# Kernel tuning notes

Hardware: AMD Instinct MI355X
Metric: run time of the kernel (lower is better)

The kernel has to match this reference:

```python
import jax, jax.numpy as jnp
import numpy as np

H, W = 512, 512
N_GAUSS = 4096
T_EPS = 1e-3          # early-termination threshold from the torch loop
COV_DIAG = 25.0       # hardcoded cov_2d = eye(2) * 25 in rasterize_gaussians


def quat_to_rot(q):
    # standard (w, x, y, z) quaternion -> rotation matrix, with normalization
    q = q / jnp.linalg.norm(q)
    w, x, y, z = q[0], q[1], q[2], q[3]
    return jnp.array([
        [1 - 2 * (y * y + z * z), 2 * (x * y - w * z),     2 * (x * z + w * y)],
        [2 * (x * y + w * z),     1 - 2 * (x * x + z * z), 2 * (y * z - w * x)],
        [2 * (x * z - w * y),     2 * (y * z + w * x),     1 - 2 * (x * x + y * y)],
    ])


def setup_inputs() -> dict:
    key = jax.random.key(0)
    k0, k1, k2, k3 = jax.random.split(key, 4)
    xy = jax.random.uniform(k0, (N_GAUSS, 2), minval=-2.0, maxval=2.0)
    z = jax.random.uniform(k1, (N_GAUSS, 1), minval=4.0, maxval=10.0)
    positions = jnp.concatenate([xy, z], axis=-1)                    # [N,3], z>0
    colors = jax.random.uniform(k2, (N_GAUSS, 3))                    # [N,3] in [0,1]
    opacities = jax.random.uniform(k3, (N_GAUSS,)) * 0.5             # [N]
    quaternion = jnp.array([1.0, 0.05, 0.02, 0.01], dtype=jnp.float32)
    cam_position = jnp.zeros(3, dtype=jnp.float32)
    intrinsics = jnp.array([[500.0, 0.0, 256.0],
                            [0.0, 500.0, 256.0],
                            [0.0, 0.0, 1.0]], dtype=jnp.float32)
    background_color = jnp.zeros(3, dtype=jnp.float32)
    return {"positions": positions, "colors": colors, "opacities": opacities,
            "quaternion": quaternion, "cam_position": cam_position,
            "intrinsics": intrinsics, "background_color": background_color}


def _render(positions, colors, opacities, quaternion, cam_position, intrinsics,
            background_color):
    R = quat_to_rot(quaternion)                                      # [3,3]
    pos_cam = (positions - cam_position[None, :]) @ R.T              # [N,3]
    proj = pos_cam @ intrinsics.T                                    # [N,3]
    screen = proj[:, :2] / proj[:, 2:3]                              # [N,2]
    depths = proj[:, 2]                                              # [N]

    order = jnp.argsort(-depths)                                     # back-to-front
    centers_s = screen[order]
    colors_s = colors[order]
    opac_s = opacities[order]
    depth_s = pos_cam[order, 2]

    yy, xx = jnp.meshgrid(jnp.arange(H, dtype=jnp.float32),
                          jnp.arange(W, dtype=jnp.float32), indexing="ij")
    pix = jnp.stack([xx, yy], axis=-1)                               # [H,W,2] (x,y)

    init_color = jnp.broadcast_to(background_color[:, None, None], (3, H, W))
    carry0 = (init_color, jnp.zeros((H, W)), jnp.zeros((H, W)), jnp.ones((H, W)))

    def step(carry, g):
        color_acc, depth_acc, alpha_acc, T = carry
        center, color, opacity, depth = g
        # emulate the `if transmittance.max() < 1e-3: break` exactly: once T
        # saturates it is monotone, so masking all later contributions == break
        active = (jnp.max(T) >= T_EPS).astype(T.dtype)
        diff = pix - center[None, None, :]                           # [H,W,2]
        mahal = jnp.sum(diff * diff, axis=-1) / COV_DIAG             # cov_inv = I/25
        alpha = jnp.clip(jnp.exp(-0.5 * mahal) * opacity, 0.0, 1.0) * active
        ta = T * alpha
        color_acc = color_acc + ta[None, :, :] * color[:, None, None]
        depth_acc = depth_acc + ta * depth
        alpha_acc = alpha_acc + ta
        T = T * (1.0 - alpha)
        return (color_acc, depth_acc, alpha_acc, T), None

    (image, depth_map, alpha_map, _), _ = jax.lax.scan(
        step, carry0, (centers_s, colors_s, opac_s, depth_s))
    return image, depth_map, alpha_map


def reference(positions, colors, opacities, quaternion, cam_position, intrinsics,
              background_color):
    return _render(positions, colors, opacities, quaternion, cam_position,
                   intrinsics, background_color)
```

## Files before the change

kernel.cpp:

```cpp
#include <hip/hip_runtime.h>
#include <hip/hip_bf16.h>

#define N_GAUSS 4096
#define H 512
#define W 512
#define HW (H * W)

#define SEG 4
#define GSEG (N_GAUSS / SEG)
#define NSUB (GSEG / 64)
#define CULL2 1444.0f
#define CAP 512


__device__ __forceinline__ float depth_key(const float* __restrict__ pos,
                                           float r20, float r21, float r22,
                                           float c0, float c1, float c2, int g) {
    float px = pos[3 * g] - c0, py = pos[3 * g + 1] - c1, pz = pos[3 * g + 2] - c2;
    return -(r20 * px + r21 * py + r22 * pz);
}

__global__ __launch_bounds__(256) void rank_partial_kernel(
        const float* __restrict__ pos, const float* __restrict__ quat,
        const float* __restrict__ cam, int* __restrict__ rankpart) {
    __shared__ __align__(16) float skj[256];
    __shared__ float ski[256];
    int t = threadIdx.x;
    int bi = blockIdx.x & 15, bj = blockIdx.x >> 4;
    float qw = quat[0], qx = quat[1], qy = quat[2], qz = quat[3];
    float qn = 1.0f / sqrtf(qw * qw + qx * qx + qy * qy + qz * qz);
    qw *= qn; qx *= qn; qy *= qn; qz *= qn;
    float r20 = 2.f * (qx * qz - qw * qy), r21 = 2.f * (qy * qz + qw * qx),
          r22 = 1.f - 2.f * (qx * qx + qy * qy);
    float c0 = cam[0], c1 = cam[1], c2 = cam[2];
    int gi = bi * 256 + t, gj = bj * 256 + t;
    ski[t] = depth_key(pos, r20, r21, r22, c0, c1, c2, gi);
    skj[t] = depth_key(pos, r20, r21, r22, c0, c1, c2, gj);
    __syncthreads();
    float ki = ski[t];
    int jbase = bj * 256;
    int r = 0;
    #pragma unroll
    for (int j = 0; j < 256; j += 4) {
        float4 k4 = *reinterpret_cast<const float4*>(&skj[j]);
        r += (k4.x < ki) || (k4.x == ki && (jbase + j + 0) < gi);
        r += (k4.y < ki) || (k4.y == ki && (jbase + j + 1) < gi);
        r += (k4.z < ki) || (k4.z == ki && (jbase + j + 2) < gi);
        r += (k4.w < ki) || (k4.w == ki && (jbase + j + 3) < gi);
    }
    rankpart[bj * N_GAUSS + gi] = r;
}

__global__ __launch_bounds__(256) void scatter_kernel(
        const float* __restrict__ pos, const float* __restrict__ quat,
        const float* __restrict__ cam, const float* __restrict__ Km,
        const float* __restrict__ colors, const float* __restrict__ opac,
        const int* __restrict__ rankpart,
        float4* __restrict__ sorted, float2* __restrict__ cxy) {
    int t = threadIdx.x;
    int i = blockIdx.x * 256 + t;
    int r = 0;
    #pragma unroll
    for (int b = 0; b < 16; ++b) r += rankpart[b * N_GAUSS + i];
    float qw = quat[0], qx = quat[1], qy = quat[2], qz = quat[3];
    float qn = 1.0f / sqrtf(qw * qw + qx * qx + qy * qy + qz * qz);
    qw *= qn; qx *= qn; qy *= qn; qz *= qn;
    float r00 = 1.f - 2.f * (qy * qy + qz * qz), r01 = 2.f * (qx * qy - qw * qz), r02 = 2.f * (qx * qz + qw * qy);
    float r10 = 2.f * (qx * qy + qw * qz), r11 = 1.f - 2.f * (qx * qx + qz * qz), r12 = 2.f * (qy * qz - qw * qx);
    float r20 = 2.f * (qx * qz - qw * qy), r21 = 2.f * (qy * qz + qw * qx), r22 = 1.f - 2.f * (qx * qx + qy * qy);
    float px = pos[3 * i] - cam[0], py = pos[3 * i + 1] - cam[1], pz = pos[3 * i + 2] - cam[2];
    float X = r00 * px + r01 * py + r02 * pz;
    float Y = r10 * px + r11 * py + r12 * pz;
    float Z = r20 * px + r21 * py + r22 * pz;
    float u = Km[0] * X + Km[1] * Y + Km[2] * Z;
    float v = Km[3] * X + Km[4] * Y + Km[5] * Z;
    float w = Km[6] * X + Km[7] * Y + Km[8] * Z;
    float sx = u / w, sy = v / w;
    sorted[2 * r]     = make_float4(sx, sy, Z, opac[i]);
    sorted[2 * r + 1] = make_float4(colors[3 * i], colors[3 * i + 1], colors[3 * i + 2], 0.f);
    cxy[r] = make_float2(sx, sy);
}

__global__ __launch_bounds__(256) void seg_render_kernel(
        const float4* __restrict__ gs, const float2* __restrict__ cxy,
        float* __restrict__ segbuf) {
    __shared__ unsigned long long smask[NSUB];
    __shared__ int sprefix[NSUB + 1];
    __shared__ unsigned short sidx[GSEG];
    __shared__ __align__(16) float4 cmp[2 * CAP];
    __shared__ int swalive[4];

    int tid = threadIdx.x;
    int lane = tid & 63, wid = tid >> 6;
    int tile = (blockIdx.x * 341) & 1023;
    int seg = blockIdx.y;
    int gbase = seg * GSEG;
    int tx0 = (tile & 31) * 16, ty0 = (tile >> 5) * 16;
    float px = (float)(tx0 + (tid & 15)), py = (float)(ty0 + (tid >> 4));
    float tcx = tx0 + 7.5f, tcy = ty0 + 7.5f;

    for (int k = 0; k < NSUB / 4; ++k) {
        int sc = k * 4 + wid;
        int g = gbase + sc * 64 + lane;
        float2 c2 = cxy[g];
        float ddx = c2.x - tcx, ddy = c2.y - tcy;
        bool pred = (ddx * ddx + ddy * ddy <= CULL2);
        unsigned long long m = __ballot(pred ? 1 : 0);
        if (pred) {
            int pos = __popcll(m & ((1ull << lane) - 1ull));
            sidx[sc * 64 + pos] = (unsigned short)g;
        }
        if (lane == 0) smask[sc] = m;
    }
    __syncthreads();

    if (wid == 0 && lane < NSUB) {
        int c = __popcll(smask[lane]);
        int inc = c;
        #pragma unroll
        for (int d = 1; d < NSUB; d <<= 1) {
            int n = __shfl_up(inc, d, 64);
            if (lane >= d) inc += n;
        }
        sprefix[lane] = inc - c;
        if (lane == NSUB - 1) sprefix[NSUB] = inc;
    }
    __syncthreads();
    int total = sprefix[NSUB];

    float T = 1.f, cr = 0.f, cg = 0.f, cb = 0.f, da = 0.f, aa = 0.f;
    bool saturated = false;

    for (int base = 0; base < total && !saturated; base += CAP) {
        int cnt = min(CAP, total - base);
        for (int s = tid; s < cnt; s += 256) {
            int gpos = base + s;
            int lo = 0, hi = NSUB;
            #pragma unroll
            for (int it = 0; it < 4; ++it) {
                int mid = (lo + hi) >> 1;
                if (sprefix[mid] <= gpos) lo = mid; else hi = mid;
            }
            int idx = sidx[lo * 64 + (gpos - sprefix[lo])];
            cmp[2 * s]     = gs[2 * idx];
            cmp[2 * s + 1] = gs[2 * idx + 1];
        }
        __syncthreads();
        #pragma unroll 2
        for (int g = 0; g < cnt; ++g) {
            float4 GA = cmp[2 * g];
            float dx = px - GA.x, dy = py - GA.y;
            float al = __expf(-0.02f * (dx * dx + dy * dy)) * GA.w;
            float ta = T * al;
            float4 GC = cmp[2 * g + 1];
            cr += ta * GC.x; cg += ta * GC.y; cb += ta * GC.z;
            da += ta * GA.z; aa += ta;
            T -= ta;
            if ((g & 127) == 127 && g + 1 < cnt) {
                unsigned long long alive = __ballot(T >= 1e-6f ? 1 : 0);
                if (lane == 0) swalive[wid] = (alive != 0ull);
                __syncthreads();
                bool allsat = !(swalive[0] | swalive[1] | swalive[2] | swalive[3]);
                __syncthreads();
                if (allsat) { saturated = true; break; }
            }
        }
        __syncthreads();
    }

    float* o = segbuf + (tile * SEG + seg) * 6 * 256 + tid;
    o[0 * 256] = cr;  o[1 * 256] = cg;  o[2 * 256] = cb;
    o[3 * 256] = da;  o[4 * 256] = aa;  o[5 * 256] = T;
}

__global__ __launch_bounds__(256) void combine_kernel(
        const float* __restrict__ segbuf, const float* __restrict__ bg,
        float* __restrict__ out) {
    int tile = blockIdx.x;
    int tid = threadIdx.x;
    const float* sb = segbuf + tile * SEG * 6 * 256 + tid;
    float r = 0.f, g = 0.f, b = 0.f, d = 0.f, a = 0.f;
    #pragma unroll
    for (int s = SEG - 1; s >= 0; --s) {
        const float* o = sb + s * 6 * 256;
        float T = o[5 * 256];
        r = o[0 * 256] + T * r;
        g = o[1 * 256] + T * g;
        b = o[2 * 256] + T * b;
        d = o[3 * 256] + T * d;
        a = o[4 * 256] + T * a;
    }
    int tx0 = (tile & 31) * 16, ty0 = (tile >> 5) * 16;
    int pid = (ty0 + (tid >> 4)) * W + tx0 + (tid & 15);
    out[pid]          = bg[0] + r;
    out[HW + pid]     = bg[1] + g;
    out[2 * HW + pid] = bg[2] + b;
    out[3 * HW + pid] = d;
    out[4 * HW + pid] = a;
}

extern "C" void kernel_launch(void* const* d_in, const int* in_sizes, int n_in,
                              void* d_out, int out_size, void* d_ws, size_t ws_size,
                              hipStream_t stream) {
    const float* positions = (const float*)d_in[0];
    const float* colors    = (const float*)d_in[1];
    const float* opacities = (const float*)d_in[2];
    const float* quat      = (const float*)d_in[3];
    const float* cam       = (const float*)d_in[4];
    const float* intr      = (const float*)d_in[5];
    const float* bg        = (const float*)d_in[6];
    float* out = (float*)d_out;

    float*  ws       = (float*)d_ws;
    float4* sorted   = (float4*)ws;
    float2* cxy      = (float2*)(ws + 32768);
    float*  segbuf   = ws + 40960;
    int*    rankpart = (int*)(ws + 6332416);

    rank_partial_kernel<<<dim3(256), dim3(256), 0, stream>>>(
        positions, quat, cam, rankpart);
    scatter_kernel<<<dim3(16), dim3(256), 0, stream>>>(
        positions, quat, cam, intr, colors, opacities, rankpart,
        sorted, cxy);
    seg_render_kernel<<<dim3(1024, SEG), dim3(256), 0, stream>>>(
        sorted, cxy, segbuf);
    combine_kernel<<<dim3(1024), dim3(256), 0, stream>>>(segbuf, bg, out);
}
```

Baseline: 116.0 us.

## Fuse segment render and combine into one 1024-thread block per tile

Merges the per-segment render kernel and the combine kernel into a single kernel where each 1024-thread block handles one tile, with four 256-thread groups each processing one depth segment. Partial results are combined in shared memory instead of a global scratch buffer, which removes one launch and the segbuf round trip. The early-saturation ballot/sync check is removed and the staging chunk shrinks to 256. All segments loop up to the max segment count with block-wide barriers, so shorter segments idle. Shared memory per block grows, which may limit occupancy.

Measured after the change: 110.5 us. 1.05x faster.

```diff
diff --git a/kernel.cpp b/kernel.cpp
--- a/kernel.cpp
+++ b/kernel.cpp
@@ -8,9 +8,8 @@
 
 #define SEG 4
 #define GSEG (N_GAUSS / SEG)
-#define NSUB (GSEG / 64)
 #define CULL2 1444.0f
-#define CAP 512
+#define CAPS 256
 
 
 __device__ __forceinline__ float depth_key(const float* __restrict__ pos,
@@ -81,27 +80,32 @@
     cxy[r] = make_float2(sx, sy);
 }
 
-__global__ __launch_bounds__(256) void seg_render_kernel(
+__global__ __launch_bounds__(1024, 8) void render_fused_kernel(
         const float4* __restrict__ gs, const float2* __restrict__ cxy,
-        float* __restrict__ segbuf) {
-    __shared__ unsigned long long smask[NSUB];
-    __shared__ int sprefix[NSUB + 1];
-    __shared__ unsigned short sidx[GSEG];
-    __shared__ __align__(16) float4 cmp[2 * CAP];
-    __shared__ int swalive[4];
+        const float* __restrict__ bg, float* __restrict__ out) {
+    __shared__ unsigned long long smask[64];
+    __shared__ int sprefix[SEG][17];
+    __shared__ unsigned short sidx[N_GAUSS];
+    __shared__ __align__(16) float4 cmp[SEG][2 * CAPS];
+    __shared__ float comb[SEG][6][256];
+    __shared__ int stmax;
 
     int tid = threadIdx.x;
-    int lane = tid & 63, wid = tid >> 6;
+    int lane = tid & 63;
+    int wave = tid >> 6;
+    int seg = wave >> 2;
+    int lw = wave & 3;
+    int p = tid & 255;
     int tile = (blockIdx.x * 341) & 1023;
-    int seg = blockIdx.y;
-    int gbase = seg * GSEG;
     int tx0 = (tile & 31) * 16, ty0 = (tile >> 5) * 16;
-    float px = (float)(tx0 + (tid & 15)), py = (float)(ty0 + (tid >> 4));
+    float px = (float)(tx0 + (p & 15)), py = (float)(ty0 + (p >> 4));
     float tcx = tx0 + 7.5f, tcy = ty0 + 7.5f;
 
-    for (int k = 0; k < NSUB / 4; ++k) {
-        int sc = k * 4 + wid;
-        int g = gbase + sc * 64 + lane;
+    if (tid == 0) stmax = 0;
+
+    for (int k = 0; k < 4; ++k) {
+        int sc = seg * 16 + lw * 4 + k;
+        int g = sc * 64 + lane;
         float2 c2 = cxy[g];
         float ddx = c2.x - tcx, ddy = c2.y - tcy;
         bool pred = (ddx * ddx + ddy * ddy <= CULL2);
@@ -114,89 +118,76 @@
     }
     __syncthreads();
 
-    if (wid == 0 && lane < NSUB) {
-        int c = __popcll(smask[lane]);
+    if (lw == 0 && lane < 16) {
+        int c = __popcll(smask[seg * 16 + lane]);
         int inc = c;
         #pragma unroll
-        for (int d = 1; d < NSUB; d <<= 1) {
+        for (int d = 1; d < 16; d <<= 1) {
             int n = __shfl_up(inc, d, 64);
             if (lane >= d) inc += n;
         }
-        sprefix[lane] = inc - c;
-        if (lane == NSUB - 1) sprefix[NSUB] = inc;
-    }
-    __syncthreads();
-    int total = sprefix[NSUB];
+        sprefix[seg][lane] = inc - c;
+        if (lane == 15) {
+            sprefix[seg][16] = inc;
+            atomicMax(&stmax, inc);
+        }
+    }
+    __syncthreads();
+    int total = sprefix[seg][16];
+    int tmax = stmax;
 
     float T = 1.f, cr = 0.f, cg = 0.f, cb = 0.f, da = 0.f, aa = 0.f;
-    bool saturated = false;
-
-    for (int base = 0; base < total && !saturated; base += CAP) {
-        int cnt = min(CAP, total - base);
-        for (int s = tid; s < cnt; s += 256) {
+
+    for (int base = 0; base < tmax; base += CAPS) {
+        int cnt = min(CAPS, total - base);
+        for (int s = p; s < cnt; s += 256) {
             int gpos = base + s;
-            int lo = 0, hi = NSUB;
+            int lo = 0, hi = 16;
             #pragma unroll
             for (int it = 0; it < 4; ++it) {
                 int mid = (lo + hi) >> 1;
-                if (sprefix[mid] <= gpos) lo = mid; else hi = mid;
+                if (sprefix[seg][mid] <= gpos) lo = mid; else hi = mid;
             }
-            int idx = sidx[lo * 64 + (gpos - sprefix[lo])];
-            cmp[2 * s]     = gs[2 * idx];
-            cmp[2 * s + 1] = gs[2 * idx + 1];
+            int idx = sidx[(seg * 16 + lo) * 64 + (gpos - sprefix[seg][lo])];
+            cmp[seg][2 * s]     = gs[2 * idx];
+            cmp[seg][2 * s + 1] = gs[2 * idx + 1];
         }
         __syncthreads();
         #pragma unroll 2
         for (int g = 0; g < cnt; ++g) {
-            float4 GA = cmp[2 * g];
+            float4 GA = cmp[seg][2 * g];
             float dx = px - GA.x, dy = py - GA.y;
             float al = __expf(-0.02f * (dx * dx + dy * dy)) * GA.w;
             float ta = T * al;
-            float4 GC = cmp[2 * g + 1];
+            float4 GC = cmp[seg][2 * g + 1];
             cr += ta * GC.x; cg += ta * GC.y; cb += ta * GC.z;
             da += ta * GA.z; aa += ta;
             T -= ta;
-            if ((g & 127) == 127 && g + 1 < cnt) {
-                unsigned long long alive = __ballot(T >= 1e-6f ? 1 : 0);
-                if (lane == 0) swalive[wid] = (alive != 0ull);
-                __syncthreads();
-                bool allsat = !(swalive[0] | swalive[1] | swalive[2] | swalive[3]);
-                __syncthreads();
-                if (allsat) { saturated = true; break; }
-            }
         }
         __syncthreads();
     }
 
-    float* o = segbuf + (tile * SEG + seg) * 6 * 256 + tid;
-    o[0 * 256] = cr;  o[1 * 256] = cg;  o[2 * 256] = cb;
-    o[3 * 256] = da;  o[4 * 256] = aa;  o[5 * 256] = T;
-}
-
-__global__ __launch_bounds__(256) void combine_kernel(
-        const float* __restrict__ segbuf, const float* __restrict__ bg,
-        float* __restrict__ out) {
-    int tile = blockIdx.x;
-    int tid = threadIdx.x;
-    const float* sb = segbuf + tile * SEG * 6 * 256 + tid;
-    float r = 0.f, g = 0.f, b = 0.f, d = 0.f, a = 0.f;
-    #pragma unroll
-    for (int s = SEG - 1; s >= 0; --s) {
-        const float* o = sb + s * 6 * 256;
-        float T = o[5 * 256];
-        r = o[0 * 256] + T * r;
-        g = o[1 * 256] + T * g;
-        b = o[2 * 256] + T * b;
-        d = o[3 * 256] + T * d;
-        a = o[4 * 256] + T * a;
-    }
-    int tx0 = (tile & 31) * 16, ty0 = (tile >> 5) * 16;
-    int pid = (ty0 + (tid >> 4)) * W + tx0 + (tid & 15);
-    out[pid]          = bg[0] + r;
-    out[HW + pid]     = bg[1] + g;
-    out[2 * HW + pid] = bg[2] + b;
-    out[3 * HW + pid] = d;
-    out[4 * HW + pid] = a;
+    comb[seg][0][p] = cr;  comb[seg][1][p] = cg;  comb[seg][2][p] = cb;
+    comb[seg][3][p] = da;  comb[seg][4][p] = aa;  comb[seg][5][p] = T;
+    __syncthreads();
+    if (seg == 0) {
+        float r = 0.f, g2 = 0.f, b = 0.f, d = 0.f, a = 0.f;
+        #pragma unroll
+        for (int s = SEG - 1; s >= 0; --s) {
+            float Ts = comb[s][5][p];
+            r  = comb[s][0][p] + Ts * r;
+            g2 = comb[s][1][p] + Ts * g2;
+            b  = comb[s][2][p] + Ts * b;
+            d  = comb[s][3][p] + Ts * d;
+            a  = comb[s][4][p] + Ts * a;
+        }
+        int pid = (ty0 + (p >> 4)) * W + tx0 + (p & 15);
+        out[pid]          = bg[0] + r;
+        out[HW + pid]     = bg[1] + g2;
+        out[2 * HW + pid] = bg[2] + b;
+        out[3 * HW + pid] = d;
+        out[4 * HW + pid] = a;
+    }
 }
 
 extern "C" void kernel_launch(void* const* d_in, const int* in_sizes, int n_in,
@@ -214,15 +205,13 @@
     float*  ws       = (float*)d_ws;
     float4* sorted   = (float4*)ws;
     float2* cxy      = (float2*)(ws + 32768);
-    float*  segbuf   = ws + 40960;
-    int*    rankpart = (int*)(ws + 6332416);
+    int*    rankpart = (int*)(ws + 49152);
 
     rank_partial_kernel<<<dim3(256), dim3(256), 0, stream>>>(
         positions, quat, cam, rankpart);
     scatter_kernel<<<dim3(16), dim3(256), 0, stream>>>(
         positions, quat, cam, intr, colors, opacities, rankpart,
         sorted, cxy);
-    seg_render_kernel<<<dim3(1024, SEG), dim3(256), 0, stream>>>(
-        sorted, cxy, segbuf);
-    combine_kernel<<<dim3(1024), dim3(256), 0, stream>>>(segbuf, bg, out);
-}
+    render_fused_kernel<<<dim3(1024), dim3(1024), 0, stream>>>(
+        sorted, cxy, bg, out);
+}
```
